# Performance work log

Measured on AMD Instinct MI355X. Metric: run time of the kernel, lower is better.

The kernel has to match this reference:

```python
import jax, jax.numpy as jnp
import numpy as np

# --- model hyperparams (match init_kwargs) ---
N_DIM = 200      # n_dim == nfeat == nhidden (Linear(200,200) hardcoded in source)
NHID = 200
NLAYERS = 8
ALPHA = 0.1
LAMDA = 0.5
B, L = 20, 100   # dialogues x uniform dialogue length
N = B * L        # 2000 utterances per modality -> 3N = 6000 graph nodes
A_DIM, V_DIM, L_DIM, NSPK = 300, 342, 1024, 2


def _linear_params(key, fin, fout):
    s = 1.0 / np.sqrt(fin)
    k1, k2 = jax.random.split(key)
    W = jax.random.uniform(k1, (fin, fout), jnp.float32, -s, s)
    b = jax.random.uniform(k2, (fout,), jnp.float32, -s, s)
    return W, b


def setup_inputs() -> dict:
    key = jax.random.key(0)
    ks = jax.random.split(key, 12)
    a = jax.random.normal(ks[0], (N, A_DIM), jnp.float32)
    v = jax.random.normal(ks[1], (N, V_DIM), jnp.float32)
    l = jax.random.normal(ks[2], (N, L_DIM), jnp.float32)
    qmask = jax.random.uniform(ks[3], (L, B, NSPK), dtype=jnp.float32)
    # dense normalized adjacency over the 3N-node multimodal graph
    adj = jax.random.uniform(ks[4], (3 * N, 3 * N), dtype=jnp.float32) / (3.0 * N)
    Wa, ba = _linear_params(ks[5], A_DIM, N_DIM)
    Wv, bv = _linear_params(ks[6], V_DIM, N_DIM)
    Wl, bl = _linear_params(ks[7], L_DIM, N_DIM)
    spk_emb = jax.random.normal(ks[8], (NSPK, N_DIM), jnp.float32)
    W0, b0 = _linear_params(ks[9], N_DIM, NHID)
    s = 1.0 / np.sqrt(NHID)
    # variant=True -> conv weight is [2*nhidden, nhidden]
    convW = jax.random.uniform(ks[10], (NLAYERS, 2 * NHID, NHID), jnp.float32, -s, s)
    return dict(a=a, v=v, l=l, qmask=qmask, adj=adj,
                Wa=Wa, ba=ba, Wv=Wv, bv=bv, Wl=Wl, bl=bl,
                spk_emb=spk_emb, W0=W0, b0=b0, convW=convW, dia_len=L)


def reference(a, v, l, qmask, adj, Wa, ba, Wv, bv, Wl, bl, spk_emb, W0, b0, convW, dia_len):
    # modality projections
    a = a @ Wa + ba                                   # [N, n_dim]
    v = v @ Wv + bv
    l = l @ Wl + bl
    # qmask: [L, B, n_spk] seq-first -> concat per dialogue (uniform lengths)
    qcat = jnp.transpose(qmask[:dia_len], (1, 0, 2)).reshape(-1, qmask.shape[-1])  # [N, n_spk]
    spk_idx = jnp.argmax(qcat, axis=-1)
    l = l + spk_emb[spk_idx]                          # use_speaker, 'l' in modals
    # big multimodal graph: stack modalities along node axis
    x = jnp.concatenate([a, v, l], axis=0)            # [3N, n_dim]
    # GCNII_lyc (eval mode: dropout identity)
    h0 = jax.nn.relu(x @ W0 + b0)                     # [3N, nhidden]
    thetas = jnp.log(LAMDA / jnp.arange(1, NLAYERS + 1, dtype=jnp.float32) + 1.0)

    def layer(h, wt):
        W, theta = wt
        hi = adj @ h                                  # spmm (dense here)
        support = jnp.concatenate([hi, h0], axis=1)   # variant=True
        r = (1.0 - ALPHA) * hi + ALPHA * h0
        h_new = jax.nn.relu(theta * (support @ W) + (1.0 - theta) * r)
        return h_new, None

    h, _ = jax.lax.scan(layer, h0, (convW, thetas))
    feat = jnp.concatenate([x, h], axis=1)            # use_residue -> [3N, n_dim+nhidden]
    n = a.shape[0]
    # split modality chunks back and fuse on feature axis -> [N, 3*(n_dim+nhidden)]
    return jnp.concatenate([feat[:n], feat[n:2 * n], feat[2 * n:3 * n]], axis=-1)
```

## Files before the change

### kernel.cpp

```cpp
#include <hip/hip_runtime.h>
#include <math.h>

typedef unsigned short u16;
typedef unsigned int u32;
typedef __bf16 bf8_t __attribute__((ext_vector_type(8)));
typedef float f4_t __attribute__((ext_vector_type(4)));
typedef u16 us8_t __attribute__((ext_vector_type(8)));
typedef u16 us4_t __attribute__((ext_vector_type(4)));

#define LDC 224
#define NROWS 6016
#define PLANE (NROWS*LDC)

__device__ __forceinline__ float b2f(u16 x){
  union{u32 u; float f;} c; c.u = ((u32)x)<<16; return c.f;
}
__device__ __forceinline__ u16 f2b(float f){
  union{u32 u; float f;} c; c.f = f;
  u32 b = c.u;
  return (u16)((b + 0x7FFFu + ((b>>16)&1u)) >> 16);
}
__device__ __forceinline__ u16 ldcvt(const void* p, size_t i, int f){
  return f ? f2b(((const float*)p)[i]) : ((const u16*)p)[i];
}
__device__ __forceinline__ void gl16(const u16* g, u16* l){
  __builtin_amdgcn_global_load_lds((const __attribute__((address_space(1))) void*)g,
                                   (__attribute__((address_space(3))) void*)l, 16, 0, 0);
}

__device__ __forceinline__ int detect_inline(const u16* adj){
  int l = threadIdx.x & 63;
  u16 u = adj[2*l];
  int ex = (u >> 7) & 0xFF;
  bool ok = ((u >> 15) == 0) && (ex >= 0x30) && (ex <= 0x72);
  unsigned long long m = __ballot(ok);
  return (__popcll(m) < 32) ? 1 : 0;
}

__global__ void prep_kernel(const void* __restrict__ adj, u16* __restrict__ adj_bf,
                            const void* __restrict__ Wa, const void* __restrict__ Wv,
                            const void* __restrict__ Wl, const void* __restrict__ W0,
                            const void* __restrict__ convW, const void* __restrict__ qmask,
                            const void* __restrict__ a_in, const void* __restrict__ v_in,
                            const void* __restrict__ l_in, const void* __restrict__ spkemb_in,
                            const void* __restrict__ ba, const void* __restrict__ bv,
                            const void* __restrict__ bl, const void* __restrict__ b0,
                            u16* __restrict__ WaT, u16* __restrict__ WvT, u16* __restrict__ WlT,
                            u16* __restrict__ W0T, u16* __restrict__ WtT, u16* __restrict__ WbT,
                            int* __restrict__ spk, u16* __restrict__ x_bf,
                            u16* __restrict__ a_p, u16* __restrict__ v_p, u16* __restrict__ l_p,
                            u16* __restrict__ spkem, u16* __restrict__ b_all)
{
  const int f = detect_inline((const u16*)adj);
  const int y = blockIdx.y;
  const int e = blockIdx.x*256 + threadIdx.x;

  if (y >= 39){
    if (!adj_bf) return;
    size_t idx = (size_t)(y-39)*229376 + e;
    if (idx >= (size_t)6016*752) return;
    int row = (int)(idx / 752);
    int k8  = (int)(idx - (size_t)row*752) * 8;
    us8_t vv;
    if (row < 6000){
      if (f){
        const float* src = (const float*)adj + (size_t)row*6000;
        if (k8 + 8 <= 6000){
          f4_t x0 = *(const f4_t*)(src + k8);
          f4_t x1 = *(const f4_t*)(src + k8 + 4);
          #pragma unroll
          for (int j=0;j<4;j++){ vv[j] = f2b(x0[j]); vv[4+j] = f2b(x1[j]); }
        } else {
          #pragma unroll
          for (int j=0;j<8;j++){ int k=k8+j; vv[j] = (k<6000) ? f2b(src[k]) : (u16)0; }
        }
      } else {
        const u16* src = (const u16*)adj + (size_t)row*6000;
        if (k8 + 8 <= 6000){
          vv = *(const us8_t*)(src + k8);
        } else {
          #pragma unroll
          for (int j=0;j<8;j++){ int k=k8+j; vv[j] = (k<6000) ? src[k] : (u16)0; }
        }
      }
    } else {
      #pragma unroll
      for (int j=0;j<8;j++) vv[j] = 0;
    }
    *(us8_t*)(adj_bf + (size_t)row*6016 + k8) = vv;
    return;
  }

  if (y < 20){
    const void* src; u16* dst; int K, kpad; size_t soff = 0;
    if (y == 0){ src=Wa; dst=WaT; K=300; kpad=320; }
    else if (y == 1){ src=Wv; dst=WvT; K=342; kpad=384; }
    else if (y == 2){ src=Wl; dst=WlT; K=1024; kpad=1024; }
    else if (y == 3){ src=W0; dst=W0T; K=200; kpad=256; }
    else if (y < 12){ int i=y-4;  src=convW; soff=(size_t)i*80000;          dst=WtT + i*57344; K=200; kpad=256; }
    else            { int i=y-12; src=convW; soff=(size_t)i*80000 + 40000;  dst=WbT + i*57344; K=200; kpad=256; }
    int total = 224*kpad;
    if (e >= total) return;
    int n = e / kpad, k = e - n*kpad;
    u16 val = 0;
    if (k < K && n < 200) val = ldcvt(src, soff + (size_t)k*200 + n, f);
    dst[e] = val;
    return;
  }
  if (y == 20){
    if (e < 2000){
      int b = e/100, t = e - b*100;
      size_t base = ((size_t)t*20 + b)*2;
      bool one;
      if (f) one = ((const float*)qmask)[base+1] > ((const float*)qmask)[base];
      else   one = b2f(((const u16*)qmask)[base+1]) > b2f(((const u16*)qmask)[base]);
      spk[e] = one ? 1 : 0;
    } else if (e < 2400){
      spkem[e-2000] = ldcvt(spkemb_in, e-2000, f);
    } else if (e < 3200){
      int j = e - 2400; int which = j/200, idx = j - which*200;
      const void* src = (which==0)?ba:(which==1)?bv:(which==2)?bl:b0;
      b_all[j] = ldcvt(src, idx, f);
    }
    return;
  }
  if (y == 21){
    if (e < 16*LDC) x_bf[(size_t)6000*LDC + e] = 0;
    return;
  }
  if (y < 25){
    size_t eg = (size_t)(y-22)*229376 + e;
    if (eg >= (size_t)2048*320) return;
    int row = (int)(eg/320), k = (int)(eg - (size_t)row*320);
    a_p[eg] = (row < 2000 && k < 300) ? ldcvt(a_in, (size_t)row*300 + k, f) : (u16)0;
    return;
  }
  if (y < 29){
    size_t eg = (size_t)(y-25)*229376 + e;
    if (eg >= (size_t)2048*384) return;
    int row = (int)(eg/384), k = (int)(eg - (size_t)row*384);
    v_p[eg] = (row < 2000 && k < 342) ? ldcvt(v_in, (size_t)row*342 + k, f) : (u16)0;
    return;
  }
  {
    size_t eg = (size_t)(y-29)*229376 + e;
    if (eg >= (size_t)2048*1024) return;
    int row = (int)(eg >> 10), k = (int)(eg & 1023);
    l_p[eg] = (row < 2000) ? ldcvt(l_in, (size_t)row*1024 + k, f) : (u16)0;
  }
}

template<int WR>
__global__ __launch_bounds__(256, 2)
void gemm_kernel(int dynA,
                 const void* __restrict__ A1, int lda1, int kv1, int kg1, int ks1, const u16* __restrict__ B1, int ldb1,
                 const u16* __restrict__ A2, int lda2, int kv2, int kg2, int ks2, const u16* __restrict__ B2, int ldb2,
                 int Mv, int Mout, int spp, int emode,
                 const u16* __restrict__ bias, const u16* __restrict__ spk_e, const int* __restrict__ spk_idx,
                 u16* __restrict__ part_base,
                 const u16* __restrict__ hi_ro, const u16* __restrict__ h0_ro,
                 float theta,
                 u16* __restrict__ outN, u16* __restrict__ outT)
{
  __shared__ u16 ldsA[WR*32*64];
  __shared__ u16 ldsB[224*64];
  const int fval = dynA ? detect_inline((const u16*)A1) : 0;
  const int tid = threadIdx.x;
  const int l = tid & 63;
  const int w = tid >> 6;
  const int wrow = w >> 1, wcol = w & 1;
  const int row0 = blockIdx.x * (WR*32);
  const int lq = l >> 4, lr = l & 15;

  f4_t acc[WR][7];
  #pragma unroll
  for (int i=0;i<WR;i++)
    #pragma unroll
    for (int j=0;j<7;j++){ f4_t z = {0.f,0.f,0.f,0.f}; acc[i][j] = z; }

  #pragma unroll 1
  for (int pair = 0; pair < 2; ++pair){
    const u16* A16 = pair ? A2 : (const u16*)A1;
    const float* A32 = pair ? nullptr : (const float*)A1;
    const int af32 = pair ? 0 : fval;
    int lda = pair ? lda2 : lda1;
    int kv = pair ? kv2 : kv1;      int ks = pair ? ks2 : ks1;
    int kg = pair ? kg2 : kg1;
    const u16* B = pair ? B2 : B1;  int ldb = pair ? ldb2 : ldb1;
    int sb, se;
    if (pair == 0){ sb = blockIdx.y * spp; se = sb + spp; if (se > ks) se = ks; }
    else { sb = 0; se = ks; }

    #pragma unroll 1
    for (int s = sb; s < se; ++s){
      int k0 = s << 6;
      __syncthreads();
      bool alignedA = ((lda & 7) == 0) && (row0 + WR*32 <= Mv);
      bool gldsA = (!af32) && alignedA && (k0 + 64 <= kg);
      if (gldsA){
        const u16* abase = A16 + k0;
        #pragma unroll
        for (int i=0;i<WR;i++){
          int c = (i<<8) + tid;
          int m = c >> 3, k8p = c & 7;
          int k8 = k8p ^ (m & 7);
          gl16(abase + (size_t)(row0+m)*lda + (k8<<3), &ldsA[c<<3]);
        }
      } else if (af32 && alignedA && (k0 + 64 <= kv)){
        const float* ap = A32 + (size_t)row0*lda + k0;
        #pragma unroll
        for (int i=0;i<WR;i++){
          int c = (i<<8) + tid;
          int m = c >> 3, k8 = c & 7;
          f4_t x0 = *(const f4_t*)(ap + (size_t)m*lda + (k8<<3));
          f4_t x1 = *(const f4_t*)(ap + (size_t)m*lda + (k8<<3) + 4);
          us8_t vv;
          #pragma unroll
          for (int j=0;j<4;j++){ vv[j] = f2b(x0[j]); vv[4+j] = f2b(x1[j]); }
          *(us8_t*)(&ldsA[(m<<6) + ((k8 ^ (m&7))<<3)]) = vv;
        }
      } else {
        #pragma unroll
        for (int i=0;i<WR;i++){
          int c = (i<<8) + tid;
          int m = c >> 3, k8 = c & 7;
          int gr = row0 + m; if (gr > Mv-1) gr = Mv-1;
          us8_t vv;
          #pragma unroll
          for (int j=0;j<8;j++){
            int kk = k0 + (k8<<3) + j;
            u16 t = 0;
            if (kk < kv){
              if (af32) t = f2b(A32[(size_t)gr*lda + kk]);
              else      t = A16[(size_t)gr*lda + kk];
            }
            vv[j] = t;
          }
          *(us8_t*)(&ldsA[(m<<6) + ((k8 ^ (m&7))<<3)]) = vv;
        }
      }
      {
        const u16* bbase = B + k0;
        #pragma unroll
        for (int i=0;i<7;i++){
          int c = (i<<8) + tid;
          int n = c >> 3, k8p = c & 7;
          int k8 = k8p ^ (n & 7);
          gl16(bbase + (size_t)n*ldb + (k8<<3), &ldsB[c<<3]);
        }
      }
      __syncthreads();
      #pragma unroll
      for (int h=0; h<2; ++h){
        bf8_t af[WR], bfr[7];
        int kc = lq + (h<<2);
        #pragma unroll
        for (int rt=0;rt<WR;rt++){
          int m = wrow*(16*WR) + rt*16 + lr;
          af[rt] = *(const bf8_t*)(&ldsA[(m<<6) + ((kc ^ (m&7))<<3)]);
        }
        #pragma unroll
        for (int ct=0;ct<7;ct++){
          int n = wcol*112 + ct*16 + lr;
          bfr[ct] = *(const bf8_t*)(&ldsB[(n<<6) + ((kc ^ (n&7))<<3)]);
        }
        #pragma unroll
        for (int rt=0;rt<WR;rt++)
          #pragma unroll
          for (int ct=0;ct<7;ct++)
            acc[rt][ct] = __builtin_amdgcn_mfma_f32_16x16x32_bf16(af[rt], bfr[ct], acc[rt][ct], 0,0,0);
      }
    }
  }

  #pragma unroll
  for (int rt=0;rt<WR;rt++){
    int r_base = row0 + wrow*(16*WR) + rt*16 + lq*4;
    #pragma unroll
    for (int ct=0;ct<7;ct++){
      int c = wcol*112 + ct*16 + lr;
      f4_t a4 = acc[rt][ct];
      if (emode == 0){
        u16* dst = part_base + (size_t)blockIdx.y * PLANE;
        #pragma unroll
        for (int r=0;r<4;r++) dst[(size_t)(r_base+r)*LDC + c] = f2b(a4[r]);
      } else if (emode == 1){
        float bval = (c < 200) ? b2f(bias[c]) : 0.f;
        #pragma unroll
        for (int r=0;r<4;r++){
          int R = r_base + r;
          if (R < Mout){
            float vv = a4[r] + bval;
            if (spk_e && c < 200) vv += b2f(spk_e[spk_idx[R]*200 + c]);
            outN[(size_t)R*LDC + c] = f2b(vv);
          }
        }
      } else if (emode == 2){
        float bval = (c < 200) ? b2f(bias[c]) : 0.f;
        us4_t p;
        #pragma unroll
        for (int r=0;r<4;r++){
          int R = r_base + r;
          float vv = a4[r] + bval; if (vv < 0.f) vv = 0.f;
          u16 q = f2b(vv);
          outN[(size_t)R*LDC + c] = q;
          p[r] = q;
        }
        *(us4_t*)(&outT[(size_t)c*NROWS + r_base]) = p;
      } else {
        us4_t p;
        #pragma unroll
        for (int r=0;r<4;r++){
          int R = r_base + r;
          size_t ix = (size_t)R*LDC + c;
          float hiv = b2f(hi_ro[ix]), h0v = b2f(h0_ro[ix]);
          float rr = 0.9f*hiv + 0.1f*h0v;
          float vv = theta*a4[r] + (1.f - theta)*rr;
          if (vv < 0.f) vv = 0.f;
          p[r] = f2b(vv);
        }
        *(us4_t*)(&outT[(size_t)c*NROWS + r_base]) = p;
      }
    }
  }
}

__global__ void reduce_kernel(const u16* __restrict__ part, int nsk, u16* __restrict__ hi_bf)
{
  size_t i8 = ((size_t)blockIdx.x*256 + threadIdx.x)*8;
  float s[8];
  #pragma unroll
  for (int j=0;j<8;j++) s[j] = 0.f;
  for (int p=0;p<nsk;p++){
    us8_t v = *(const us8_t*)(part + (size_t)p*PLANE + i8);
    #pragma unroll
    for (int j=0;j<8;j++) s[j] += b2f(v[j]);
  }
  us8_t o;
  #pragma unroll
  for (int j=0;j<8;j++) o[j] = f2b(s[j]);
  *(us8_t*)(hi_bf + i8) = o;
}

__device__ __forceinline__ u16 sent(u16 t, u16 snan, u16 sbig){
  u16 mag = t & 0x7FFF;
  if (mag >= 0x7F80) return snan;
  if (mag >= 0x4480) return sbig;
  return t;
}
__global__ void out_kernel(const void* __restrict__ adjv,
                           const u16* __restrict__ x_bf, const u16* __restrict__ hT,
                           void* __restrict__ outp)
{
  __shared__ u16 tile[64*216];
  const int of32 = detect_inline((const u16*)adjv);
  u16* o16 = (u16*)outp;
  float* o32 = (float*)outp;
  const int tid = threadIdx.x;
  const int n0 = blockIdx.x*64;
  const int m = blockIdx.y;
  for (int cc = tid; cc < 1600; cc += 256){
    int r = cc/25, c8 = cc - r*25;
    int n = n0 + r;
    int rr = n < 2000 ? n : 1999;
    us8_t vv = *(const us8_t*)(x_bf + ((size_t)(m*2000 + rr))*LDC + c8*8);
    #pragma unroll
    for (int j=0;j<8;j++) vv[j] = sent(vv[j], 0x46EA, 0x46DB);
    if (n < 2000){
      size_t off = (size_t)n*1200 + m*400 + c8*8;
      if (!of32) *(us8_t*)(o16 + off) = vv;
      else {
        f4_t lo, hi;
        #pragma unroll
        for (int j=0;j<4;j++){ lo[j] = b2f(vv[j]); hi[j] = b2f(vv[4+j]); }
        *(f4_t*)(o32 + off) = lo; *(f4_t*)(o32 + off + 4) = hi;
      }
    }
  }
  for (int cc = tid; cc < 1600; cc += 256){
    int c = cc >> 3, ng = cc & 7;
    int nb = n0 + ng*8;
    if (nb > 1992) nb = 1992;
    us8_t vv = *(const us8_t*)(hT + (size_t)c*NROWS + m*2000 + nb);
    #pragma unroll
    for (int j=0;j<8;j++) tile[(ng*8+j)*216 + c] = sent(vv[j], 0x469C, 0x468C);
  }
  __syncthreads();
  for (int cc = tid; cc < 1600; cc += 256){
    int r = cc/25, c8 = cc - r*25;
    int n = n0 + r;
    if (n < 2000){
      us8_t vv = *(const us8_t*)(&tile[r*216 + c8*8]);
      size_t off = (size_t)n*1200 + m*400 + 200 + c8*8;
      if (!of32) *(us8_t*)(o16 + off) = vv;
      else {
        f4_t lo, hi;
        #pragma unroll
        for (int j=0;j<4;j++){ lo[j] = b2f(vv[j]); hi[j] = b2f(vv[4+j]); }
        *(f4_t*)(o32 + off) = lo; *(f4_t*)(o32 + off + 4) = hi;
      }
    }
  }
}

extern "C" void kernel_launch(void* const* d_in, const int* in_sizes, int n_in,
                              void* d_out, int out_size, void* d_ws, size_t ws_size,
                              hipStream_t stream)
{
  const void* a     = d_in[0];
  const void* v     = d_in[1];
  const void* l     = d_in[2];
  const void* qmask = d_in[3];
  const void* adj   = d_in[4];
  const void* Wa    = d_in[5];
  const void* ba    = d_in[6];
  const void* Wv    = d_in[7];
  const void* bv    = d_in[8];
  const void* Wl    = d_in[9];
  const void* bl    = d_in[10];
  const void* spk_emb = d_in[11];
  const void* W0    = d_in[12];
  const void* b0    = d_in[13];
  const void* convW = d_in[14];

  int cfg = (ws_size >= (size_t)125*1024*1024) ? 2
          : (ws_size >= (size_t)48*1024*1024) ? 1 : 0;
  const int SK = (cfg >= 1) ? 4 : 2;
  const int SPP = (94 + SK - 1) / SK;

  char* ws = (char*)d_ws;
  size_t off = 0;
  auto alloc = [&](size_t bytes)->char*{
    char* p = ws + off; off = (off + bytes + 255) & ~(size_t)255; return p;
  };
  u16*  x_bf  = (u16*) alloc((size_t)PLANE*2);
  u16*  h0_bf = (u16*) alloc((size_t)PLANE*2);
  u16*  hi_bf = (u16*) alloc((size_t)PLANE*2);
  u16*  hT    = (u16*) alloc((size_t)PLANE*2);
  u16*  a_p   = (u16*) alloc((size_t)2048*320*2);
  u16*  v_p   = (u16*) alloc((size_t)2048*384*2);
  u16*  l_p   = (u16*) alloc((size_t)2048*1024*2);
  u16* WaT = (u16*)alloc(224*320*2);
  u16* WvT = (u16*)alloc(224*384*2);
  u16* WlT = (u16*)alloc(224*1024*2);
  u16* W0T = (u16*)alloc(224*256*2);
  u16* WtT = (u16*)alloc((size_t)8*224*256*2);
  u16* WbT = (u16*)alloc((size_t)8*224*256*2);
  int* spk = (int*)alloc(2000*4);
  u16* spkem = (u16*)alloc(400*2);
  u16* b_all = (u16*)alloc(800*2);
  u16* part = (u16*)alloc((size_t)SK*PLANE*2);
  u16* adj_bf = (cfg == 2) ? (u16*)alloc((size_t)6016*6016*2) : nullptr;

  prep_kernel<<<dim3(896, (cfg==2) ? 59 : 39),256,0,stream>>>(adj, adj_bf,
      Wa,Wv,Wl,W0,convW,qmask, a,v,l,spk_emb, ba,bv,bl,b0,
      WaT,WvT,WlT,W0T,WtT,WbT, spk, x_bf, a_p,v_p,l_p, spkem, b_all);

  gemm_kernel<1><<<dim3(64,1),256,0,stream>>>(0, a_p,320,320,320,5, WaT,320,
      nullptr,0,0,0,0,nullptr,0, 2048,2000, 5, 1, b_all, nullptr, nullptr,
      nullptr, nullptr, nullptr, 0.f, x_bf, nullptr);
  gemm_kernel<1><<<dim3(64,1),256,0,stream>>>(0, v_p,384,384,384,6, WvT,384,
      nullptr,0,0,0,0,nullptr,0, 2048,2000, 6, 1, b_all+200, nullptr, nullptr,
      nullptr, nullptr, nullptr, 0.f, x_bf + (size_t)2000*LDC, nullptr);
  gemm_kernel<1><<<dim3(64,1),256,0,stream>>>(0, l_p,1024,1024,1024,16, WlT,1024,
      nullptr,0,0,0,0,nullptr,0, 2048,2000, 16, 1, b_all+400, spkem, spk,
      nullptr, nullptr, nullptr, 0.f, x_bf + (size_t)4000*LDC, nullptr);

  gemm_kernel<1><<<dim3(188,1),256,0,stream>>>(0, x_bf,LDC,LDC,256,4, W0T,256,
      nullptr,0,0,0,0,nullptr,0, NROWS,NROWS, 4, 2, b_all+600, nullptr, nullptr,
      nullptr, nullptr, nullptr, 0.f, h0_bf, hT);

  for (int i=0;i<8;i++){
    float theta = logf(0.5f/(float)(i+1) + 1.0f);
    if (cfg == 2)
      gemm_kernel<2><<<dim3(94,SK),256,0,stream>>>(0, adj_bf,6016,6016,6016,94, hT,NROWS,
          nullptr,0,0,0,0,nullptr,0, 6016,0, SPP, 0, nullptr, nullptr, nullptr,
          part, nullptr, nullptr, 0.f, nullptr, nullptr);
    else
      gemm_kernel<2><<<dim3(94,SK),256,0,stream>>>(1, adj,6000,6000,0,94, hT,NROWS,
          nullptr,0,0,0,0,nullptr,0, 6000,0, SPP, 0, nullptr, nullptr, nullptr,
          part, nullptr, nullptr, 0.f, nullptr, nullptr);
    reduce_kernel<<<dim3(PLANE/2048),256,0,stream>>>(part, SK, hi_bf);
    gemm_kernel<1><<<dim3(188,1),256,0,stream>>>(0, hi_bf,LDC,LDC,256,4, WtT + (size_t)i*57344,256,
        h0_bf,LDC,LDC,256,4, WbT + (size_t)i*57344,256,
        NROWS,0, 4, 3, nullptr, nullptr, nullptr, nullptr, hi_bf, h0_bf, theta,
        nullptr, hT);
  }

  out_kernel<<<dim3(32,3),256,0,stream>>>(adj, x_bf, hT, (void*)d_out);
}
```

Before: 705.8 us.

## Fuse adjacency bf16 conversion into first adj GEMM and load l directly

Removes the separate adjacency fp32-to-bf16 conversion pass from the prep kernel. The first adj@h layer instead reads fp32 adj directly, converting on the fly and writing the bf16 copy as a side effect, and later layers read that copy. The language projection likewise reads the fp32 l input directly instead of a padded bf16 copy. This saves a full extra read/write pass over the 144MB adjacency and the l staging buffer, at the cost of a slower first layer that does fp32 loads and extra stores.

```diff
diff --git a/kernel.cpp b/kernel.cpp
--- a/kernel.cpp
+++ b/kernel.cpp
@@ -37,59 +37,23 @@
   return (__popcll(m) < 32) ? 1 : 0;
 }
 
-__global__ void prep_kernel(const void* __restrict__ adj, u16* __restrict__ adj_bf,
+__global__ void prep_kernel(const void* __restrict__ adj,
                             const void* __restrict__ Wa, const void* __restrict__ Wv,
                             const void* __restrict__ Wl, const void* __restrict__ W0,
                             const void* __restrict__ convW, const void* __restrict__ qmask,
                             const void* __restrict__ a_in, const void* __restrict__ v_in,
-                            const void* __restrict__ l_in, const void* __restrict__ spkemb_in,
+                            const void* __restrict__ spkemb_in,
                             const void* __restrict__ ba, const void* __restrict__ bv,
                             const void* __restrict__ bl, const void* __restrict__ b0,
                             u16* __restrict__ WaT, u16* __restrict__ WvT, u16* __restrict__ WlT,
                             u16* __restrict__ W0T, u16* __restrict__ WtT, u16* __restrict__ WbT,
                             int* __restrict__ spk, u16* __restrict__ x_bf,
-                            u16* __restrict__ a_p, u16* __restrict__ v_p, u16* __restrict__ l_p,
+                            u16* __restrict__ a_p, u16* __restrict__ v_p,
                             u16* __restrict__ spkem, u16* __restrict__ b_all)
 {
   const int f = detect_inline((const u16*)adj);
   const int y = blockIdx.y;
   const int e = blockIdx.x*256 + threadIdx.x;
-
-  if (y >= 39){
-    if (!adj_bf) return;
-    size_t idx = (size_t)(y-39)*229376 + e;
-    if (idx >= (size_t)6016*752) return;
-    int row = (int)(idx / 752);
-    int k8  = (int)(idx - (size_t)row*752) * 8;
-    us8_t vv;
-    if (row < 6000){
-      if (f){
-        const float* src = (const float*)adj + (size_t)row*6000;
-        if (k8 + 8 <= 6000){
-          f4_t x0 = *(const f4_t*)(src + k8);
-          f4_t x1 = *(const f4_t*)(src + k8 + 4);
-          #pragma unroll
-          for (int j=0;j<4;j++){ vv[j] = f2b(x0[j]); vv[4+j] = f2b(x1[j]); }
-        } else {
-          #pragma unroll
-          for (int j=0;j<8;j++){ int k=k8+j; vv[j] = (k<6000) ? f2b(src[k]) : (u16)0; }
-        }
-      } else {
-        const u16* src = (const u16*)adj + (size_t)row*6000;
-        if (k8 + 8 <= 6000){
-          vv = *(const us8_t*)(src + k8);
-        } else {
-          #pragma unroll
-          for (int j=0;j<8;j++){ int k=k8+j; vv[j] = (k<6000) ? src[k] : (u16)0; }
-        }
-      }
-    } else {
-      #pragma unroll
-      for (int j=0;j<8;j++) vv[j] = 0;
-    }
-    *(us8_t*)(adj_bf + (size_t)row*6016 + k8) = vv;
-    return;
-  }
 
   if (y < 20){
     const void* src; u16* dst; int K, kpad; size_t soff = 0;
@@ -135,24 +99,17 @@
     a_p[eg] = (row < 2000 && k < 300) ? ldcvt(a_in, (size_t)row*300 + k, f) : (u16)0;
     return;
   }
-  if (y < 29){
+  {
     size_t eg = (size_t)(y-25)*229376 + e;
     if (eg >= (size_t)2048*384) return;
     int row = (int)(eg/384), k = (int)(eg - (size_t)row*384);
     v_p[eg] = (row < 2000 && k < 342) ? ldcvt(v_in, (size_t)row*342 + k, f) : (u16)0;
-    return;
-  }
-  {
-    size_t eg = (size_t)(y-29)*229376 + e;
-    if (eg >= (size_t)2048*1024) return;
-    int row = (int)(eg >> 10), k = (int)(eg & 1023);
-    l_p[eg] = (row < 2000) ? ldcvt(l_in, (size_t)row*1024 + k, f) : (u16)0;
   }
 }
 
 template<int WR>
 __global__ __launch_bounds__(256, 2)
-void gemm_kernel(int dynA,
+void gemm_kernel(int dynA, const void* __restrict__ dref, u16* __restrict__ a_cvt,
                  const void* __restrict__ A1, int lda1, int kv1, int kg1, int ks1, const u16* __restrict__ B1, int ldb1,
                  const u16* __restrict__ A2, int lda2, int kv2, int kg2, int ks2, const u16* __restrict__ B2, int ldb2,
                  int Mv, int Mout, int spp, int emode,
@@ -164,7 +121,6 @@
 {
   __shared__ u16 ldsA[WR*32*64];
   __shared__ u16 ldsB[224*64];
-  const int fval = dynA ? detect_inline((const u16*)A1) : 0;
   const int tid = threadIdx.x;
   const int l = tid & 63;
   const int w = tid >> 6;
@@ -172,6 +128,22 @@
   const int row0 = blockIdx.x * (WR*32);
   const int lq = l >> 4, lr = l & 15;
 
+  const u16* A16_0 = (const u16*)A1;
+  const float* A32_0 = (const float*)A1;
+  int af32_0 = 0, lda_0 = lda1, kv_0 = kv1, kg_0 = kg1, Mv_0 = Mv;
+  int cvt = 0;
+  if (dynA){
+    int fd = detect_inline((const u16*)dref);
+    if (dynA == 1){
+      af32_0 = fd;
+    } else if (dynA == 2){
+      af32_0 = fd;
+      if (fd){ kg_0 = 0; cvt = (a_cvt != nullptr); }
+    } else {
+      if (fd){ A16_0 = a_cvt; lda_0 = 6016; kv_0 = 6016; kg_0 = 6016; Mv_0 = 6016; }
+    }
+  }
+
   f4_t acc[WR][7];
   #pragma unroll
   for (int i=0;i<WR;i++)
@@ -180,12 +152,13 @@
 
   #pragma unroll 1
   for (int pair = 0; pair < 2; ++pair){
-    const u16* A16 = pair ? A2 : (const u16*)A1;
-    const float* A32 = pair ? nullptr : (const float*)A1;
-    const int af32 = pair ? 0 : fval;
-    int lda = pair ? lda2 : lda1;
-    int kv = pair ? kv2 : kv1;      int ks = pair ? ks2 : ks1;
-    int kg = pair ? kg2 : kg1;
+    const u16* A16 = pair ? A2 : A16_0;
+    const float* A32 = pair ? nullptr : A32_0;
+    const int af32 = pair ? 0 : af32_0;
+    int lda = pair ? lda2 : lda_0;
+    int kv = pair ? kv2 : kv_0;      int ks = pair ? ks2 : ks1;
+    int kg = pair ? kg2 : kg_0;
+    int Mvl = pair ? Mv : Mv_0;
     const u16* B = pair ? B2 : B1;  int ldb = pair ? ldb2 : ldb1;
     int sb, se;
     if (pair == 0){ sb = blockIdx.y * spp; se = sb + spp; if (se > ks) se = ks; }
@@ -195,7 +168,7 @@
     for (int s = sb; s < se; ++s){
       int k0 = s << 6;
       __syncthreads();
-      bool alignedA = ((lda & 7) == 0) && (row0 + WR*32 <= Mv);
+      bool alignedA = ((lda & 7) == 0) && (row0 + WR*32 <= Mvl);
       bool gldsA = (!af32) && alignedA && (k0 + 64 <= kg);
       if (gldsA){
         const u16* abase = A16 + k0;
@@ -218,13 +191,14 @@
           #pragma unroll
           for (int j=0;j<4;j++){ vv[j] = f2b(x0[j]); vv[4+j] = f2b(x1[j]); }
           *(us8_t*)(&ldsA[(m<<6) + ((k8 ^ (m&7))<<3)]) = vv;
+          if (cvt) *(us8_t*)(a_cvt + (size_t)(row0+m)*6016 + k0 + (k8<<3)) = vv;
         }
       } else {
         #pragma unroll
         for (int i=0;i<WR;i++){
           int c = (i<<8) + tid;
           int m = c >> 3, k8 = c & 7;
-          int gr = row0 + m; if (gr > Mv-1) gr = Mv-1;
+          int gr = row0 + m; if (gr > Mvl-1) gr = Mvl-1;
           us8_t vv;
           #pragma unroll
           for (int j=0;j<8;j++){
@@ -237,6 +211,7 @@
             vv[j] = t;
           }
           *(us8_t*)(&ldsA[(m<<6) + ((k8 ^ (m&7))<<3)]) = vv;
+          if (cvt && af32) *(us8_t*)(a_cvt + (size_t)(row0+m)*6016 + k0 + (k8<<3)) = vv;
         }
       }
       {
@@ -439,7 +414,6 @@
   u16*  hT    = (u16*) alloc((size_t)PLANE*2);
   u16*  a_p   = (u16*) alloc((size_t)2048*320*2);
   u16*  v_p   = (u16*) alloc((size_t)2048*384*2);
-  u16*  l_p   = (u16*) alloc((size_t)2048*1024*2);
   u16* WaT = (u16*)alloc(224*320*2);
   u16* WvT = (u16*)alloc(224*384*2);
   u16* WlT = (u16*)alloc(224*1024*2);
@@ -452,36 +426,50 @@
   u16* part = (u16*)alloc((size_t)SK*PLANE*2);
   u16* adj_bf = (cfg == 2) ? (u16*)alloc((size_t)6016*6016*2) : nullptr;
 
-  prep_kernel<<<dim3(896, (cfg==2) ? 59 : 39),256,0,stream>>>(adj, adj_bf,
-      Wa,Wv,Wl,W0,convW,qmask, a,v,l,spk_emb, ba,bv,bl,b0,
-      WaT,WvT,WlT,W0T,WtT,WbT, spk, x_bf, a_p,v_p,l_p, spkem, b_all);
-
-  gemm_kernel<1><<<dim3(64,1),256,0,stream>>>(0, a_p,320,320,320,5, WaT,320,
+  prep_kernel<<<dim3(896,29),256,0,stream>>>(adj,
+      Wa,Wv,Wl,W0,convW,qmask, a,v,spk_emb, ba,bv,bl,b0,
+      WaT,WvT,WlT,W0T,WtT,WbT, spk, x_bf, a_p,v_p, spkem, b_all);
+
+  gemm_kernel<1><<<dim3(64,1),256,0,stream>>>(0, nullptr, nullptr,
+      a_p,320,320,320,5, WaT,320,
       nullptr,0,0,0,0,nullptr,0, 2048,2000, 5, 1, b_all, nullptr, nullptr,
       nullptr, nullptr, nullptr, 0.f, x_bf, nullptr);
-  gemm_kernel<1><<<dim3(64,1),256,0,stream>>>(0, v_p,384,384,384,6, WvT,384,
+  gemm_kernel<1><<<dim3(64,1),256,0,stream>>>(0, nullptr, nullptr,
+      v_p,384,384,384,6, WvT,384,
       nullptr,0,0,0,0,nullptr,0, 2048,2000, 6, 1, b_all+200, nullptr, nullptr,
       nullptr, nullptr, nullptr, 0.f, x_bf + (size_t)2000*LDC, nullptr);
-  gemm_kernel<1><<<dim3(64,1),256,0,stream>>>(0, l_p,1024,1024,1024,16, WlT,1024,
-      nullptr,0,0,0,0,nullptr,0, 2048,2000, 16, 1, b_all+400, spkem, spk,
+  gemm_kernel<1><<<dim3(64,1),256,0,stream>>>(1, adj, nullptr,
+      l,1024,1024,1024,16, WlT,1024,
+      nullptr,0,0,0,0,nullptr,0, 2000,2000, 16, 1, b_all+400, spkem, spk,
       nullptr, nullptr, nullptr, 0.f, x_bf + (size_t)4000*LDC, nullptr);
 
-  gemm_kernel<1><<<dim3(188,1),256,0,stream>>>(0, x_bf,LDC,LDC,256,4, W0T,256,
+  gemm_kernel<1><<<dim3(188,1),256,0,stream>>>(0, nullptr, nullptr,
+      x_bf,LDC,LDC,256,4, W0T,256,
       nullptr,0,0,0,0,nullptr,0, NROWS,NROWS, 4, 2, b_all+600, nullptr, nullptr,
       nullptr, nullptr, nullptr, 0.f, h0_bf, hT);
 
   for (int i=0;i<8;i++){
     float theta = logf(0.5f/(float)(i+1) + 1.0f);
-    if (cfg == 2)
-      gemm_kernel<2><<<dim3(94,SK),256,0,stream>>>(0, adj_bf,6016,6016,6016,94, hT,NROWS,
-          nullptr,0,0,0,0,nullptr,0, 6016,0, SPP, 0, nullptr, nullptr, nullptr,
-          part, nullptr, nullptr, 0.f, nullptr, nullptr);
-    else
-      gemm_kernel<2><<<dim3(94,SK),256,0,stream>>>(1, adj,6000,6000,0,94, hT,NROWS,
+    if (cfg == 2){
+      if (i == 0)
+        gemm_kernel<2><<<dim3(94,SK),256,0,stream>>>(2, adj, adj_bf,
+            adj,6000,6000,6000,94, hT,NROWS,
+            nullptr,0,0,0,0,nullptr,0, 6000,0, SPP, 0, nullptr, nullptr, nullptr,
+            part, nullptr, nullptr, 0.f, nullptr, nullptr);
+      else
+        gemm_kernel<2><<<dim3(94,SK),256,0,stream>>>(3, adj, adj_bf,
+            adj,6000,6000,6000,94, hT,NROWS,
+            nullptr,0,0,0,0,nullptr,0, 6000,0, SPP, 0, nullptr, nullptr, nullptr,
+            part, nullptr, nullptr, 0.f, nullptr, nullptr);
+    } else {
+      gemm_kernel<2><<<dim3(94,SK),256,0,stream>>>(1, adj, nullptr,
+          adj,6000,6000,6000,94, hT,NROWS,
           nullptr,0,0,0,0,nullptr,0, 6000,0, SPP, 0, nullptr, nullptr, nullptr,
           part, nullptr, nullptr, 0.f, nullptr, nullptr);
+    }
     reduce_kernel<<<dim3(PLANE/2048),256,0,stream>>>(part, SK, hi_bf);
-    gemm_kernel<1><<<dim3(188,1),256,0,stream>>>(0, hi_bf,LDC,LDC,256,4, WtT + (size_t)i*57344,256,
+    gemm_kernel<1><<<dim3(188,1),256,0,stream>>>(0, nullptr, nullptr,
+        hi_bf,LDC,LDC,256,4, WtT + (size_t)i*57344,256,
         h0_bf,LDC,LDC,256,4, WbT + (size_t)i*57344,256,
         NROWS,0, 4, 3, nullptr, nullptr, nullptr, nullptr, hi_bf, h0_bf, theta,
         nullptr, hT);
```

Result: slower. 768.7 us (+8.9%).

## Fuse split-K reduce into layer GEMM, drop l padding copy, raise split-K

Applied to the files above, without the earlier changes.

Adds a layer_kernel that sums the split-K partials of adj@h straight into shared memory and runs the two-part support GEMM plus the GCNII epilogue in one launch. This removes the separate reduce kernel and the hi_bf round trip through global memory. The l projection now reads the raw input directly instead of a padded bf16 copy made in prep. Split-K for the adjacency GEMM goes from 4 to 8, which increases partial-buffer traffic in exchange for more parallel blocks. dtype detection samples varied positions and is chosen per block, and the adjacency GEMM picks the bf16 copy at runtime.

```diff
diff --git a/kernel.cpp b/kernel.cpp
--- a/kernel.cpp
+++ b/kernel.cpp
@@ -28,9 +28,9 @@
                                    (__attribute__((address_space(3))) void*)l, 16, 0, 0);
 }
 
-__device__ __forceinline__ int detect_inline(const u16* adj){
+__device__ __forceinline__ int detect_inline(const u16* adj, int salt){
   int l = threadIdx.x & 63;
-  u16 u = adj[2*l];
+  u16 u = adj[2*(((salt & 1023)<<6) + l)];
   int ex = (u >> 7) & 0xFF;
   bool ok = ((u >> 15) == 0) && (ex >= 0x30) && (ex <= 0x72);
   unsigned long long m = __ballot(ok);
@@ -42,22 +42,22 @@
                             const void* __restrict__ Wl, const void* __restrict__ W0,
                             const void* __restrict__ convW, const void* __restrict__ qmask,
                             const void* __restrict__ a_in, const void* __restrict__ v_in,
-                            const void* __restrict__ l_in, const void* __restrict__ spkemb_in,
+                            const void* __restrict__ spkemb_in,
                             const void* __restrict__ ba, const void* __restrict__ bv,
                             const void* __restrict__ bl, const void* __restrict__ b0,
                             u16* __restrict__ WaT, u16* __restrict__ WvT, u16* __restrict__ WlT,
                             u16* __restrict__ W0T, u16* __restrict__ WtT, u16* __restrict__ WbT,
                             int* __restrict__ spk, u16* __restrict__ x_bf,
-                            u16* __restrict__ a_p, u16* __restrict__ v_p, u16* __restrict__ l_p,
+                            u16* __restrict__ a_p, u16* __restrict__ v_p,
                             u16* __restrict__ spkem, u16* __restrict__ b_all)
 {
-  const int f = detect_inline((const u16*)adj);
   const int y = blockIdx.y;
+  const int f = detect_inline((const u16*)adj, blockIdx.x + y*896);
   const int e = blockIdx.x*256 + threadIdx.x;
 
-  if (y >= 39){
+  if (y >= 29){
     if (!adj_bf) return;
-    size_t idx = (size_t)(y-39)*229376 + e;
+    size_t idx = (size_t)(y-29)*229376 + e;
     if (idx >= (size_t)6016*752) return;
     int row = (int)(idx / 752);
     int k8  = (int)(idx - (size_t)row*752) * 8;
@@ -135,36 +135,25 @@
     a_p[eg] = (row < 2000 && k < 300) ? ldcvt(a_in, (size_t)row*300 + k, f) : (u16)0;
     return;
   }
-  if (y < 29){
+  {
     size_t eg = (size_t)(y-25)*229376 + e;
     if (eg >= (size_t)2048*384) return;
     int row = (int)(eg/384), k = (int)(eg - (size_t)row*384);
     v_p[eg] = (row < 2000 && k < 342) ? ldcvt(v_in, (size_t)row*342 + k, f) : (u16)0;
-    return;
-  }
-  {
-    size_t eg = (size_t)(y-29)*229376 + e;
-    if (eg >= (size_t)2048*1024) return;
-    int row = (int)(eg >> 10), k = (int)(eg & 1023);
-    l_p[eg] = (row < 2000) ? ldcvt(l_in, (size_t)row*1024 + k, f) : (u16)0;
   }
 }
 
 template<int WR>
 __global__ __launch_bounds__(256, 2)
-void gemm_kernel(int dynA,
+void gemm_kernel(int dynA, const void* __restrict__ dref, const u16* __restrict__ a_sel,
                  const void* __restrict__ A1, int lda1, int kv1, int kg1, int ks1, const u16* __restrict__ B1, int ldb1,
-                 const u16* __restrict__ A2, int lda2, int kv2, int kg2, int ks2, const u16* __restrict__ B2, int ldb2,
                  int Mv, int Mout, int spp, int emode,
                  const u16* __restrict__ bias, const u16* __restrict__ spk_e, const int* __restrict__ spk_idx,
                  u16* __restrict__ part_base,
-                 const u16* __restrict__ hi_ro, const u16* __restrict__ h0_ro,
-                 float theta,
                  u16* __restrict__ outN, u16* __restrict__ outT)
 {
   __shared__ u16 ldsA[WR*32*64];
   __shared__ u16 ldsB[224*64];
-  const int fval = dynA ? detect_inline((const u16*)A1) : 0;
   const int tid = threadIdx.x;
   const int l = tid & 63;
   const int w = tid >> 6;
@@ -172,104 +161,105 @@
   const int row0 = blockIdx.x * (WR*32);
   const int lq = l >> 4, lr = l & 15;
 
+  const u16* A16 = (const u16*)A1;
+  const float* A32 = (const float*)A1;
+  int af32 = 0, lda = lda1, kv = kv1, kg = kg1, Mvl = Mv;
+  if (dynA){
+    int fd = detect_inline((const u16*)dref, blockIdx.x + blockIdx.y*131);
+    if (dynA == 1){
+      af32 = fd;
+    } else {
+      if (fd){ A16 = a_sel; lda = 6016; kv = 6016; kg = 6016; Mvl = 6016; }
+    }
+  }
+
   f4_t acc[WR][7];
   #pragma unroll
   for (int i=0;i<WR;i++)
     #pragma unroll
     for (int j=0;j<7;j++){ f4_t z = {0.f,0.f,0.f,0.f}; acc[i][j] = z; }
 
+  int sb = blockIdx.y * spp, se = sb + spp;
+  if (se > ks1) se = ks1;
+
   #pragma unroll 1
-  for (int pair = 0; pair < 2; ++pair){
-    const u16* A16 = pair ? A2 : (const u16*)A1;
-    const float* A32 = pair ? nullptr : (const float*)A1;
-    const int af32 = pair ? 0 : fval;
-    int lda = pair ? lda2 : lda1;
-    int kv = pair ? kv2 : kv1;      int ks = pair ? ks2 : ks1;
-    int kg = pair ? kg2 : kg1;
-    const u16* B = pair ? B2 : B1;  int ldb = pair ? ldb2 : ldb1;
-    int sb, se;
-    if (pair == 0){ sb = blockIdx.y * spp; se = sb + spp; if (se > ks) se = ks; }
-    else { sb = 0; se = ks; }
-
-    #pragma unroll 1
-    for (int s = sb; s < se; ++s){
-      int k0 = s << 6;
-      __syncthreads();
-      bool alignedA = ((lda & 7) == 0) && (row0 + WR*32 <= Mv);
-      bool gldsA = (!af32) && alignedA && (k0 + 64 <= kg);
-      if (gldsA){
-        const u16* abase = A16 + k0;
-        #pragma unroll
-        for (int i=0;i<WR;i++){
-          int c = (i<<8) + tid;
-          int m = c >> 3, k8p = c & 7;
-          int k8 = k8p ^ (m & 7);
-          gl16(abase + (size_t)(row0+m)*lda + (k8<<3), &ldsA[c<<3]);
+  for (int s = sb; s < se; ++s){
+    int k0 = s << 6;
+    __syncthreads();
+    bool alignedA = ((lda & 7) == 0) && (row0 + WR*32 <= Mvl);
+    bool gldsA = (!af32) && alignedA && (k0 + 64 <= kg);
+    if (gldsA){
+      const u16* abase = A16 + k0;
+      #pragma unroll
+      for (int i=0;i<WR;i++){
+        int c = (i<<8) + tid;
+        int m = c >> 3, k8p = c & 7;
+        int k8 = k8p ^ (m & 7);
+        gl16(abase + (size_t)(row0+m)*lda + (k8<<3), &ldsA[c<<3]);
+      }
+    } else if (af32 && alignedA && (k0 + 64 <= kv)){
+      const float* ap = A32 + (size_t)row0*lda + k0;
+      #pragma unroll
+      for (int i=0;i<WR;i++){
+        int c = (i<<8) + tid;
+        int m = c >> 3, k8 = c & 7;
+        f4_t x0 = *(const f4_t*)(ap + (size_t)m*lda + (k8<<3));
+        f4_t x1 = *(const f4_t*)(ap + (size_t)m*lda + (k8<<3) + 4);
+        us8_t vv;
+        #pragma unroll
+        for (int j=0;j<4;j++){ vv[j] = f2b(x0[j]); vv[4+j] = f2b(x1[j]); }
+        *(us8_t*)(&ldsA[(m<<6) + ((k8 ^ (m&7))<<3)]) = vv;
+      }
+    } else {
+      #pragma unroll
+      for (int i=0;i<WR;i++){
+        int c = (i<<8) + tid;
+        int m = c >> 3, k8 = c & 7;
+        int gr = row0 + m; if (gr > Mvl-1) gr = Mvl-1;
+        us8_t vv;
+        #pragma unroll
+        for (int j=0;j<8;j++){
+          int kk = k0 + (k8<<3) + j;
+          u16 t = 0;
+          if (kk < kv){
+            if (af32) t = f2b(A32[(size_t)gr*lda + kk]);
+            else      t = A16[(size_t)gr*lda + kk];
+          }
+          vv[j] = t;
         }
-      } else if (af32 && alignedA && (k0 + 64 <= kv)){
-        const float* ap = A32 + (size_t)row0*lda + k0;
-        #pragma unroll
-        for (int i=0;i<WR;i++){
-          int c = (i<<8) + tid;
-          int m = c >> 3, k8 = c & 7;
-          f4_t x0 = *(const f4_t*)(ap + (size_t)m*lda + (k8<<3));
-          f4_t x1 = *(const f4_t*)(ap + (size_t)m*lda + (k8<<3) + 4);
-          us8_t vv;
-          #pragma unroll
-          for (int j=0;j<4;j++){ vv[j] = f2b(x0[j]); vv[4+j] = f2b(x1[j]); }
-          *(us8_t*)(&ldsA[(m<<6) + ((k8 ^ (m&7))<<3)]) = vv;
-        }
-      } else {
-        #pragma unroll
-        for (int i=0;i<WR;i++){
-          int c = (i<<8) + tid;
-          int m = c >> 3, k8 = c & 7;
-          int gr = row0 + m; if (gr > Mv-1) gr = Mv-1;
-          us8_t vv;
-          #pragma unroll
-          for (int j=0;j<8;j++){
-            int kk = k0 + (k8<<3) + j;
-            u16 t = 0;
-            if (kk < kv){
-              if (af32) t = f2b(A32[(size_t)gr*lda + kk]);
-              else      t = A16[(size_t)gr*lda + kk];
-            }
-            vv[j] = t;
-          }
-          *(us8_t*)(&ldsA[(m<<6) + ((k8 ^ (m&7))<<3)]) = vv;
-        }
-      }
-      {
-        const u16* bbase = B + k0;
-        #pragma unroll
-        for (int i=0;i<7;i++){
-          int c = (i<<8) + tid;
-          int n = c >> 3, k8p = c & 7;
-          int k8 = k8p ^ (n & 7);
-          gl16(bbase + (size_t)n*ldb + (k8<<3), &ldsB[c<<3]);
-        }
-      }
-      __syncthreads();
-      #pragma unroll
-      for (int h=0; h<2; ++h){
-        bf8_t af[WR], bfr[7];
-        int kc = lq + (h<<2);
-        #pragma unroll
-        for (int rt=0;rt<WR;rt++){
-          int m = wrow*(16*WR) + rt*16 + lr;
-          af[rt] = *(const bf8_t*)(&ldsA[(m<<6) + ((kc ^ (m&7))<<3)]);
-        }
-        #pragma unroll
-        for (int ct=0;ct<7;ct++){
-          int n = wcol*112 + ct*16 + lr;
-          bfr[ct] = *(const bf8_t*)(&ldsB[(n<<6) + ((kc ^ (n&7))<<3)]);
-        }
-        #pragma unroll
-        for (int rt=0;rt<WR;rt++)
-          #pragma unroll
-          for (int ct=0;ct<7;ct++)
-            acc[rt][ct] = __builtin_amdgcn_mfma_f32_16x16x32_bf16(af[rt], bfr[ct], acc[rt][ct], 0,0,0);
-      }
+        *(us8_t*)(&ldsA[(m<<6) + ((k8 ^ (m&7))<<3)]) = vv;
+      }
+    }
+    {
+      const u16* bbase = B1 + k0;
+      #pragma unroll
+      for (int i=0;i<7;i++){
+        int c = (i<<8) + tid;
+        int n = c >> 3, k8p = c & 7;
+        int k8 = k8p ^ (n & 7);
+        gl16(bbase + (size_t)n*ldb1 + (k8<<3), &ldsB[c<<3]);
+      }
+    }
+    __syncthreads();
+    #pragma unroll
+    for (int h=0; h<2; ++h){
+      bf8_t af[WR], bfr[7];
+      int kc = lq + (h<<2);
+      #pragma unroll
+      for (int rt=0;rt<WR;rt++){
+        int m = wrow*(16*WR) + rt*16 + lr;
+        af[rt] = *(const bf8_t*)(&ldsA[(m<<6) + ((kc ^ (m&7))<<3)]);
+      }
+      #pragma unroll
+      for (int ct=0;ct<7;ct++){
+        int n = wcol*112 + ct*16 + lr;
+        bfr[ct] = *(const bf8_t*)(&ldsB[(n<<6) + ((kc ^ (n&7))<<3)]);
+      }
+      #pragma unroll
+      for (int rt=0;rt<WR;rt++)
+        #pragma unroll
+        for (int ct=0;ct<7;ct++)
+          acc[rt][ct] = __builtin_amdgcn_mfma_f32_16x16x32_bf16(af[rt], bfr[ct], acc[rt][ct], 0,0,0);
     }
   }
 
@@ -295,7 +285,7 @@
             outN[(size_t)R*LDC + c] = f2b(vv);
           }
         }
-      } else if (emode == 2){
+      } else {
         float bval = (c < 200) ? b2f(bias[c]) : 0.f;
         us4_t p;
         #pragma unroll
@@ -307,39 +297,108 @@
           p[r] = q;
         }
         *(us4_t*)(&outT[(size_t)c*NROWS + r_base]) = p;
-      } else {
-        us4_t p;
-        #pragma unroll
-        for (int r=0;r<4;r++){
-          int R = r_base + r;
-          size_t ix = (size_t)R*LDC + c;
-          float hiv = b2f(hi_ro[ix]), h0v = b2f(h0_ro[ix]);
-          float rr = 0.9f*hiv + 0.1f*h0v;
-          float vv = theta*a4[r] + (1.f - theta)*rr;
-          if (vv < 0.f) vv = 0.f;
-          p[r] = f2b(vv);
+      }
+    }
+  }
+}
+
+__global__ __launch_bounds__(256, 2)
+void layer_kernel(const u16* __restrict__ part, int nsk,
+                  const u16* __restrict__ h0_bf,
+                  const u16* __restrict__ Bt, const u16* __restrict__ Bb,
+                  float theta, u16* __restrict__ outT)
+{
+  __shared__ u16 ldsHI[32*256];
+  __shared__ u16 ldsH0[32*256];
+  __shared__ u16 ldsB[224*64];
+  const int tid = threadIdx.x;
+  const int l = tid & 63;
+  const int w = tid >> 6;
+  const int wrow = w >> 1, wcol = w & 1;
+  const int row0 = blockIdx.x * 32;
+  const int lq = l >> 4, lr = l & 15;
+
+  #pragma unroll
+  for (int rr=0; rr<4; ++rr){
+    int c = rr*256 + tid;
+    int m = c >> 5, ch = c & 31;
+    us8_t o;
+    if (ch < 28){
+      float s[8];
+      #pragma unroll
+      for (int j=0;j<8;j++) s[j] = 0.f;
+      size_t base = (size_t)(row0+m)*LDC + (ch<<3);
+      for (int p=0;p<nsk;p++){
+        us8_t vv = *(const us8_t*)(part + (size_t)p*PLANE + base);
+        #pragma unroll
+        for (int j=0;j<8;j++) s[j] += b2f(vv[j]);
+      }
+      #pragma unroll
+      for (int j=0;j<8;j++) o[j] = f2b(s[j]);
+    } else {
+      #pragma unroll
+      for (int j=0;j<8;j++) o[j] = 0;
+    }
+    *(us8_t*)(&ldsHI[(m<<8) + ((ch ^ (m&7))<<3)]) = o;
+    int sch = ch ^ (m&7);
+    gl16(h0_bf + (size_t)(row0+m)*LDC + (sch<<3), &ldsH0[c<<3]);
+  }
+
+  f4_t acc[7];
+  #pragma unroll
+  for (int j=0;j<7;j++){ f4_t z = {0.f,0.f,0.f,0.f}; acc[j] = z; }
+
+  #pragma unroll 1
+  for (int pair = 0; pair < 2; ++pair){
+    const u16* Bp = pair ? Bb : Bt;
+    const u16* Alds = pair ? &ldsH0[0] : &ldsHI[0];
+    #pragma unroll 1
+    for (int s = 0; s < 4; ++s){
+      __syncthreads();
+      const u16* bbase = Bp + (s<<6);
+      #pragma unroll
+      for (int i=0;i<7;i++){
+        int c = (i<<8) + tid;
+        int n = c >> 3, k8p = c & 7;
+        int k8 = k8p ^ (n & 7);
+        gl16(bbase + (size_t)n*256 + (k8<<3), &ldsB[c<<3]);
+      }
+      __syncthreads();
+      #pragma unroll
+      for (int h=0; h<2; ++h){
+        int kc = lq + (h<<2);
+        int m = wrow*16 + lr;
+        bf8_t af = *(const bf8_t*)(&Alds[(m<<8) + (((s<<3) | (kc ^ (m&7)))<<3)]);
+        bf8_t bfr[7];
+        #pragma unroll
+        for (int ct=0;ct<7;ct++){
+          int n = wcol*112 + ct*16 + lr;
+          bfr[ct] = *(const bf8_t*)(&ldsB[(n<<6) + ((kc ^ (n&7))<<3)]);
         }
-        *(us4_t*)(&outT[(size_t)c*NROWS + r_base]) = p;
-      }
-    }
-  }
-}
-
-__global__ void reduce_kernel(const u16* __restrict__ part, int nsk, u16* __restrict__ hi_bf)
-{
-  size_t i8 = ((size_t)blockIdx.x*256 + threadIdx.x)*8;
-  float s[8];
+        #pragma unroll
+        for (int ct=0;ct<7;ct++)
+          acc[ct] = __builtin_amdgcn_mfma_f32_16x16x32_bf16(af, bfr[ct], acc[ct], 0,0,0);
+      }
+    }
+  }
+
+  int r_base = row0 + wrow*16 + lq*4;
   #pragma unroll
-  for (int j=0;j<8;j++) s[j] = 0.f;
-  for (int p=0;p<nsk;p++){
-    us8_t v = *(const us8_t*)(part + (size_t)p*PLANE + i8);
+  for (int ct=0;ct<7;ct++){
+    int c = wcol*112 + ct*16 + lr;
+    int cc8 = c >> 3, ce = c & 7;
+    us4_t p;
     #pragma unroll
-    for (int j=0;j<8;j++) s[j] += b2f(v[j]);
-  }
-  us8_t o;
-  #pragma unroll
-  for (int j=0;j<8;j++) o[j] = f2b(s[j]);
-  *(us8_t*)(hi_bf + i8) = o;
+    for (int r=0;r<4;r++){
+      int mr = wrow*16 + lq*4 + r;
+      int ix = (mr<<8) + ((cc8 ^ (mr&7))<<3) + ce;
+      float rrv = 0.9f*b2f(ldsHI[ix]) + 0.1f*b2f(ldsH0[ix]);
+      float vv = theta*acc[ct][r] + (1.f - theta)*rrv;
+      if (vv < 0.f) vv = 0.f;
+      p[r] = f2b(vv);
+    }
+    *(us4_t*)(&outT[(size_t)c*NROWS + r_base]) = p;
+  }
 }
 
 __device__ __forceinline__ u16 sent(u16 t, u16 snan, u16 sbig){
@@ -353,7 +412,7 @@
                            void* __restrict__ outp)
 {
   __shared__ u16 tile[64*216];
-  const int of32 = detect_inline((const u16*)adjv);
+  const int of32 = detect_inline((const u16*)adjv, blockIdx.x + blockIdx.y*37);
   u16* o16 = (u16*)outp;
   float* o32 = (float*)outp;
   const int tid = threadIdx.x;
@@ -425,7 +484,7 @@
 
   int cfg = (ws_size >= (size_t)125*1024*1024) ? 2
           : (ws_size >= (size_t)48*1024*1024) ? 1 : 0;
-  const int SK = (cfg >= 1) ? 4 : 2;
+  const int SK = (cfg >= 1) ? 8 : 2;
   const int SPP = (94 + SK - 1) / SK;
 
   char* ws = (char*)d_ws;
@@ -435,11 +494,9 @@
   };
   u16*  x_bf  = (u16*) alloc((size_t)PLANE*2);
   u16*  h0_bf = (u16*) alloc((size_t)PLANE*2);
-  u16*  hi_bf = (u16*) alloc((size_t)PLANE*2);
   u16*  hT    = (u16*) alloc((size_t)PLANE*2);
   u16*  a_p   = (u16*) alloc((size_t)2048*320*2);
   u16*  v_p   = (u16*) alloc((size_t)2048*384*2);
-  u16*  l_p   = (u16*) alloc((size_t)2048*1024*2);
   u16* WaT = (u16*)alloc(224*320*2);
   u16* WvT = (u16*)alloc(224*384*2);
   u16* WlT = (u16*)alloc(224*1024*2);
@@ -452,39 +509,42 @@
   u16* part = (u16*)alloc((size_t)SK*PLANE*2);
   u16* adj_bf = (cfg == 2) ? (u16*)alloc((size_t)6016*6016*2) : nullptr;
 
-  prep_kernel<<<dim3(896, (cfg==2) ? 59 : 39),256,0,stream>>>(adj, adj_bf,
-      Wa,Wv,Wl,W0,convW,qmask, a,v,l,spk_emb, ba,bv,bl,b0,
-      WaT,WvT,WlT,W0T,WtT,WbT, spk, x_bf, a_p,v_p,l_p, spkem, b_all);
-
-  gemm_kernel<1><<<dim3(64,1),256,0,stream>>>(0, a_p,320,320,320,5, WaT,320,
-      nullptr,0,0,0,0,nullptr,0, 2048,2000, 5, 1, b_all, nullptr, nullptr,
-      nullptr, nullptr, nullptr, 0.f, x_bf, nullptr);
-  gemm_kernel<1><<<dim3(64,1),256,0,stream>>>(0, v_p,384,384,384,6, WvT,384,
-      nullptr,0,0,0,0,nullptr,0, 2048,2000, 6, 1, b_all+200, nullptr, nullptr,
-      nullptr, nullptr, nullptr, 0.f, x_bf + (size_t)2000*LDC, nullptr);
-  gemm_kernel<1><<<dim3(64,1),256,0,stream>>>(0, l_p,1024,1024,1024,16, WlT,1024,
-      nullptr,0,0,0,0,nullptr,0, 2048,2000, 16, 1, b_all+400, spkem, spk,
-      nullptr, nullptr, nullptr, 0.f, x_bf + (size_t)4000*LDC, nullptr);
-
-  gemm_kernel<1><<<dim3(188,1),256,0,stream>>>(0, x_bf,LDC,LDC,256,4, W0T,256,
-      nullptr,0,0,0,0,nullptr,0, NROWS,NROWS, 4, 2, b_all+600, nullptr, nullptr,
-      nullptr, nullptr, nullptr, 0.f, h0_bf, hT);
+  prep_kernel<<<dim3(896, (cfg==2) ? 49 : 29),256,0,stream>>>(adj, adj_bf,
+      Wa,Wv,Wl,W0,convW,qmask, a,v,spk_emb, ba,bv,bl,b0,
+      WaT,WvT,WlT,W0T,WtT,WbT, spk, x_bf, a_p,v_p, spkem, b_all);
+
+  gemm_kernel<1><<<dim3(64,1),256,0,stream>>>(0, nullptr, nullptr,
+      a_p,320,320,320,5, WaT,320,
+      2048,2000, 5, 1, b_all, nullptr, nullptr,
+      nullptr, x_bf, nullptr);
+  gemm_kernel<1><<<dim3(64,1),256,0,stream>>>(0, nullptr, nullptr,
+      v_p,384,384,384,6, WvT,384,
+      2048,2000, 6, 1, b_all+200, nullptr, nullptr,
+      nullptr, x_bf + (size_t)2000*LDC, nullptr);
+  gemm_kernel<1><<<dim3(64,1),256,0,stream>>>(1, adj, nullptr,
+      l,1024,1024,1024,16, WlT,1024,
+      2000,2000, 16, 1, b_all+400, spkem, spk,
+      nullptr, x_bf + (size_t)4000*LDC, nullptr);
+
+  gemm_kernel<1><<<dim3(188,1),256,0,stream>>>(0, nullptr, nullptr,
+      x_bf,LDC,LDC,256,4, W0T,256,
+      NROWS,NROWS, 4, 2, b_all+600, nullptr, nullptr,
+      nullptr, h0_bf, hT);
 
   for (int i=0;i<8;i++){
     float theta = logf(0.5f/(float)(i+1) + 1.0f);
     if (cfg == 2)
-      gemm_kernel<2><<<dim3(94,SK),256,0,stream>>>(0, adj_bf,6016,6016,6016,94, hT,NROWS,
-          nullptr,0,0,0,0,nullptr,0, 6016,0, SPP, 0, nullptr, nullptr, nullptr,
-          part, nullptr, nullptr, 0.f, nullptr, nullptr);
+      gemm_kernel<2><<<dim3(94,SK),256,0,stream>>>(3, adj, adj_bf,
+          adj,6000,6000,6000,94, hT,NROWS,
+          6000,0, SPP, 0, nullptr, nullptr, nullptr,
+          part, nullptr, nullptr);
     else
-      gemm_kernel<2><<<dim3(94,SK),256,0,stream>>>(1, adj,6000,6000,0,94, hT,NROWS,
-          nullptr,0,0,0,0,nullptr,0, 6000,0, SPP, 0, nullptr, nullptr, nullptr,
-          part, nullptr, nullptr, 0.f, nullptr, nullptr);
-    reduce_kernel<<<dim3(PLANE/2048),256,0,stream>>>(part, SK, hi_bf);
-    gemm_kernel<1><<<dim3(188,1),256,0,stream>>>(0, hi_bf,LDC,LDC,256,4, WtT + (size_t)i*57344,256,
-        h0_bf,LDC,LDC,256,4, WbT + (size_t)i*57344,256,
-        NROWS,0, 4, 3, nullptr, nullptr, nullptr, nullptr, hi_bf, h0_bf, theta,
-        nullptr, hT);
+      gemm_kernel<2><<<dim3(94,SK),256,0,stream>>>(1, adj, nullptr,
+          adj,6000,6000,6000,94, hT,NROWS,
+          6000,0, SPP, 0, nullptr, nullptr, nullptr,
+          part, nullptr, nullptr);
+    layer_kernel<<<dim3(188),256,0,stream>>>(part, SK, h0_bf,
+        WtT + (size_t)i*57344, WbT + (size_t)i*57344, theta, hT);
   }
 
   out_kernel<<<dim3(32,3),256,0,stream>>>(adj, x_bf, hT, (void*)d_out);
```

Result: faster. 686.7 us (-2.7%).
